# Optimization experiments

Measured on AMD Instinct MI355X. Metric: run time of the kernel, lower is better.

## Reference

```python
import jax, jax.numpy as jnp
import numpy as np

H = 2048  # hidden_size
I = 2048  # input_size
B = 2048  # batch


def setup_inputs() -> dict:
    key = jax.random.key(0)
    k0, k1, k2, k3, k4, k5 = jax.random.split(key, 6)
    # bipolar-domain activations live in [-1, 1]
    inp = jax.random.uniform(k0, (B, I), jnp.float32, minval=-1.0, maxval=1.0)
    hx = jax.random.uniform(k1, (B, H), jnp.float32, minval=-1.0, maxval=1.0)
    s = 1.0 / np.sqrt(H + I)
    w_f = jax.random.normal(k2, (H, H + I), jnp.float32) * s
    b_f = jax.random.normal(k3, (H,), jnp.float32) * s
    w_n = jax.random.normal(k4, (H, H + I), jnp.float32) * s
    b_n = jax.random.normal(k5, (H,), jnp.float32) * s
    return {"input": inp, "hx": hx, "w_f": w_f, "b_f": b_f, "w_n": w_n, "b_n": b_n}


def reference(input, hx, w_f, b_f, w_n, b_n):
    # Expected-value (probability-domain) math of the unary bitstream MGU cell.
    # fg_ug_tanh: FSULinear on [hx, x]; 'hardtanh is direct pass' -> identity act.
    fg_ug_in = jnp.concatenate([hx, input], axis=1)            # [B, H+I]
    fg_in = fg_ug_in @ w_f.T + b_f                              # [B, H]
    # fg_sigmoid: FSUAdd of [fg_in, ones] with scale=None -> (x + 1) / 2
    fg = (fg_in + 1.0) * 0.5                                    # [B, H]
    # fg_hx_mul: FSUMul with static in_1_prob = hx buffer
    fg_hx = fg * hx                                             # [B, H]
    # ng_ug_tanh: FSULinear on [fg*hx, x]
    ng_ug_in = jnp.concatenate([fg_hx, input], axis=1)          # [B, H+I]
    ng = ng_ug_in @ w_n.T + b_n                                 # [B, H]
    # fg_ng_mul: dynamic FSUMul; bipolar bit-inversion (1 - bitstream) negates value
    fg_ng = fg * ng
    # hy_add: FSUAdd([ng, -fg*ng, fg*hx], scale=1) -> plain sum
    hy = ng - fg_ng + fg_hx                                     # = (1-fg)*ng + fg*hx
    return hy
```

## Files before the change

### kernel.cpp

```cpp
#include <hip/hip_runtime.h>
#include <stdint.h>


#define Hdim 2048
#define Idim 2048
#define Bdim 2048
#define Ktot 4096
#define KHALF 2048
#define NSTEP (KHALF / 64)

typedef __bf16 bf16;
typedef __bf16 bf16x8 __attribute__((ext_vector_type(8)));
typedef float  f32x4  __attribute__((ext_vector_type(4)));

__device__ __forceinline__ void gload_lds16(const bf16* g, bf16* l) {
  __builtin_amdgcn_global_load_lds(
      (const __attribute__((address_space(1))) unsigned int*)g,
      (__attribute__((address_space(3))) unsigned int*)l,
      16, 0, 0);
}

__global__ void cvt_kernel(const float* __restrict__ src, bf16* __restrict__ dst, int n8) {
  int stride = gridDim.x * blockDim.x;
  for (int i = blockIdx.x * blockDim.x + threadIdx.x; i < n8; i += stride) {
    const float4* s = (const float4*)src + (size_t)i * 2;
    float4 a = s[0], b = s[1];
    bf16x8 o;
    o[0]=(bf16)a.x; o[1]=(bf16)a.y; o[2]=(bf16)a.z; o[3]=(bf16)a.w;
    o[4]=(bf16)b.x; o[5]=(bf16)b.y; o[6]=(bf16)b.z; o[7]=(bf16)b.w;
    *((bf16x8*)dst + i) = o;
  }
}

__global__ void build_a_kernel(const float* __restrict__ hx, const float* __restrict__ x,
                               bf16* __restrict__ A1, bf16* __restrict__ A2) {
  int stride = gridDim.x * blockDim.x;
  const int n8 = Bdim * Ktot / 8;
  for (int i = blockIdx.x * blockDim.x + threadIdx.x; i < n8; i += stride) {
    int e = i * 8;
    int b = e >> 12;
    int k = e & (Ktot - 1);
    const float* src = (k < Hdim) ? (hx + (size_t)b * Hdim + k)
                                  : (x  + (size_t)b * Idim + (k - Hdim));
    const float4* s = (const float4*)src;
    float4 va = s[0], vb = s[1];
    bf16x8 o;
    o[0]=(bf16)va.x; o[1]=(bf16)va.y; o[2]=(bf16)va.z; o[3]=(bf16)va.w;
    o[4]=(bf16)vb.x; o[5]=(bf16)vb.y; o[6]=(bf16)vb.z; o[7]=(bf16)vb.w;
    *((bf16x8*)A1 + i) = o;
    if (k >= Hdim) *((bf16x8*)A2 + i) = o;
  }
}

template<int EPI>
__global__ __launch_bounds__(512)
void gemm_kernel(const bf16* __restrict__ A, const bf16* __restrict__ W,
                 const float* __restrict__ bias,
                 const float* __restrict__ hx,
                 float* __restrict__ FG,
                 bf16* __restrict__ A2,
                 float* __restrict__ OUT)
{
  __shared__ bf16 lds[2][2][2][8192];

  int bid  = blockIdx.x;
  int sbid = (bid & 7) * 32 + (bid >> 3);
  int tm = sbid >> 4, tn = sbid & 15;

  int tid  = threadIdx.x;
  int w = tid >> 6, lane = tid & 63;
  int g = w >> 2, sub = w & 3;
  int wrow = (sub >> 1) * 64;
  int wcol = (sub & 1) * 64;
  int fr = lane & 15, fq = lane >> 4;
  int swz = fr & 7;

  int gtid = sub * 64 + lane;
  int srow = gtid >> 3;
  int csrc = (gtid & 7) ^ (srow & 7);
  const bf16* pA = A + (size_t)(tm * 128 + srow) * Ktot + csrc * 8 + g * KHALF;
  const bf16* pB = W + (size_t)(tn * 128 + srow) * Ktot + csrc * 8 + g * KHALF;
  int lbase = sub * 512;

#define STAGE(buf, koff) do {                                                      \
    _Pragma("unroll")                                                              \
    for (int jj = 0; jj < 4; ++jj) {                                               \
      gload_lds16(pA + (size_t)jj * 32 * Ktot + (koff), &lds[g][buf][0][jj * 2048 + lbase]); \
      gload_lds16(pB + (size_t)jj * 32 * Ktot + (koff), &lds[g][buf][1][jj * 2048 + lbase]); \
    }                                                                              \
  } while (0)

#define READS(buf_, j_) do {                                                       \
    int ch = (((j_) * 4 + fq) ^ swz) * 8;                                          \
    _Pragma("unroll")                                                              \
    for (int m = 0; m < 4; ++m)                                                    \
      af[m] = *(const bf16x8*)&lds[g][buf_][0][(wrow + m * 16 + fr) * 64 + ch];    \
    _Pragma("unroll")                                                              \
    for (int n = 0; n < 4; ++n)                                                    \
      bv[n] = *(const bf16x8*)&lds[g][buf_][1][(wcol + n * 16 + fr) * 64 + ch];    \
  } while (0)

  f32x4 acc[4][4] = {};

  STAGE(0, 0);

  const int NW = 2 * NSTEP + 1;
  for (int win = 0; win < NW; ++win) {
    int w2 = win - g;
    bool active = (unsigned)w2 < (unsigned)(2 * NSTEP);
    int t = w2 >> 1, j = w2 & 1, buf = t & 1;
    bf16x8 af[4], bv[4];
    if (active) {
      if (j == 1) READS(buf, 1);
      else asm volatile("s_waitcnt vmcnt(0)" ::: "memory");
    }
    __builtin_amdgcn_s_barrier();
    if (active) {
      if (j == 0) {
        READS(buf, 0);
        if (t + 1 < NSTEP) STAGE(buf ^ 1, (t + 1) * 64);
      }
      __builtin_amdgcn_s_setprio(1);
      #pragma unroll
      for (int m = 0; m < 4; ++m)
        #pragma unroll
        for (int n = 0; n < 4; ++n)
          acc[m][n] = __builtin_amdgcn_mfma_f32_16x16x32_bf16(af[m], bv[n], acc[m][n], 0, 0, 0);
      __builtin_amdgcn_s_setprio(0);
    }
  }
#undef STAGE
#undef READS

  __syncthreads();
  float* xch = (float*)&lds[0][0][0][0];
  if (g == 1) {
    #pragma unroll
    for (int m = 0; m < 4; ++m)
      #pragma unroll
      for (int n = 0; n < 4; ++n)
        *(f32x4*)&xch[sub * 4096 + (m * 4 + n) * 256 + lane * 4] = acc[m][n];
  }
  __syncthreads();
  if (g == 0) {
    int row0 = tm * 128 + wrow + fq * 4;
    int col0 = tn * 128 + wcol + fr;
    #pragma unroll
    for (int n = 0; n < 4; ++n) {
      int gcol = col0 + n * 16;
      float bv = bias[gcol];
      #pragma unroll
      for (int m = 0; m < 4; ++m) {
        f32x4 part = *(const f32x4*)&xch[sub * 4096 + (m * 4 + n) * 256 + lane * 4];
        #pragma unroll
        for (int i = 0; i < 4; ++i) {
          int grow = row0 + m * 16 + i;
          size_t idx = (size_t)grow * Hdim + gcol;
          float v = acc[m][n][i] + part[i] + bv;
          if (EPI == 0) {
            float fg   = (v + 1.0f) * 0.5f;
            float fghx = fg * hx[idx];
            FG[idx] = fg;
            A2[(size_t)grow * Ktot + gcol] = (bf16)fghx;
          } else {
            float fg   = FG[idx];
            float fghx = (float)A2[(size_t)grow * Ktot + gcol];
            OUT[idx] = v - fg * v + fghx;
          }
        }
      }
    }
  }
}

extern "C" void kernel_launch(void* const* d_in, const int* in_sizes, int n_in,
                              void* d_out, int out_size, void* d_ws, size_t ws_size,
                              hipStream_t stream) {
  const float* x   = (const float*)d_in[0];
  const float* hx  = (const float*)d_in[1];
  const float* w_f = (const float*)d_in[2];
  const float* b_f = (const float*)d_in[3];
  const float* w_n = (const float*)d_in[4];
  const float* b_n = (const float*)d_in[5];
  float* out = (float*)d_out;

  bf16* A1 = (bf16*)d_ws;
  bf16* A2 = A1 + (size_t)Bdim * Ktot;
  bf16* Wf = A2 + (size_t)Bdim * Ktot;
  bf16* Wn = Wf + (size_t)Hdim * Ktot;

  const int n8w = Hdim * Ktot / 8;
  cvt_kernel<<<1024, 256, 0, stream>>>(w_f, Wf, n8w);
  cvt_kernel<<<1024, 256, 0, stream>>>(w_n, Wn, n8w);
  build_a_kernel<<<1024, 256, 0, stream>>>(hx, x, A1, A2);

  gemm_kernel<0><<<256, 512, 0, stream>>>(A1, Wf, b_f, hx, out, A2, nullptr);
  gemm_kernel<1><<<256, 512, 0, stream>>>(A2, Wn, b_n, nullptr, out, A2, out);
}
```

Baseline: 117.9 us.

## Fuse prep kernels, drop duplicated x copy, store 1-fg as bf16

Merges the three fp32-to-bf16 conversion launches into one prep kernel. The second GEMM now reads the x half of its A operand straight from A1 instead of a duplicated copy, and reads the fg*hx half from a compact half-width buffer. The forget gate is kept as bf16 (1-fg) rather than fp32 fg, which cuts epilogue traffic and workspace. This removes two launches and several MB of writes and reads, but storing 1-fg in bf16 adds some rounding error.

```diff
diff --git a/kernel.cpp b/kernel.cpp
--- a/kernel.cpp
+++ b/kernel.cpp
@@ -20,45 +20,46 @@
       16, 0, 0);
 }
 
-__global__ void cvt_kernel(const float* __restrict__ src, bf16* __restrict__ dst, int n8) {
+__global__ void prep_kernel(const float* __restrict__ w_f, const float* __restrict__ w_n,
+                            const float* __restrict__ hx, const float* __restrict__ x,
+                            bf16* __restrict__ Wf, bf16* __restrict__ Wn,
+                            bf16* __restrict__ A1) {
+  const int n8 = Hdim * Ktot / 8;
   int stride = gridDim.x * blockDim.x;
-  for (int i = blockIdx.x * blockDim.x + threadIdx.x; i < n8; i += stride) {
-    const float4* s = (const float4*)src + (size_t)i * 2;
-    float4 a = s[0], b = s[1];
-    bf16x8 o;
-    o[0]=(bf16)a.x; o[1]=(bf16)a.y; o[2]=(bf16)a.z; o[3]=(bf16)a.w;
-    o[4]=(bf16)b.x; o[5]=(bf16)b.y; o[6]=(bf16)b.z; o[7]=(bf16)b.w;
-    *((bf16x8*)dst + i) = o;
-  }
-}
-
-__global__ void build_a_kernel(const float* __restrict__ hx, const float* __restrict__ x,
-                               bf16* __restrict__ A1, bf16* __restrict__ A2) {
-  int stride = gridDim.x * blockDim.x;
-  const int n8 = Bdim * Ktot / 8;
-  for (int i = blockIdx.x * blockDim.x + threadIdx.x; i < n8; i += stride) {
-    int e = i * 8;
-    int b = e >> 12;
-    int k = e & (Ktot - 1);
-    const float* src = (k < Hdim) ? (hx + (size_t)b * Hdim + k)
-                                  : (x  + (size_t)b * Idim + (k - Hdim));
+  for (int i = blockIdx.x * blockDim.x + threadIdx.x; i < 3 * n8; i += stride) {
+    const float* src;
+    bf16* dst;
+    if (i < n8) {
+      src = w_f + (size_t)i * 8;  dst = Wf + (size_t)i * 8;
+    } else if (i < 2 * n8) {
+      int j = i - n8;
+      src = w_n + (size_t)j * 8;  dst = Wn + (size_t)j * 8;
+    } else {
+      int j = i - 2 * n8;
+      int e = j * 8;
+      int b = e >> 12;
+      int k = e & (Ktot - 1);
+      src = (k < Hdim) ? (hx + (size_t)b * Hdim + k)
+                       : (x  + (size_t)b * Idim + (k - Hdim));
+      dst = A1 + (size_t)e;
+    }
     const float4* s = (const float4*)src;
     float4 va = s[0], vb = s[1];
     bf16x8 o;
     o[0]=(bf16)va.x; o[1]=(bf16)va.y; o[2]=(bf16)va.z; o[3]=(bf16)va.w;
     o[4]=(bf16)vb.x; o[5]=(bf16)vb.y; o[6]=(bf16)vb.z; o[7]=(bf16)vb.w;
-    *((bf16x8*)A1 + i) = o;
-    if (k >= Hdim) *((bf16x8*)A2 + i) = o;
+    *((bf16x8*)dst) = o;
   }
 }
 
 template<int EPI>
 __global__ __launch_bounds__(512)
-void gemm_kernel(const bf16* __restrict__ A, const bf16* __restrict__ W,
+void gemm_kernel(const bf16* __restrict__ A1, const bf16* __restrict__ A2L,
+                 const bf16* __restrict__ W,
                  const float* __restrict__ bias,
                  const float* __restrict__ hx,
-                 float* __restrict__ FG,
-                 bf16* __restrict__ A2,
+                 bf16* __restrict__ OMF,
+                 bf16* __restrict__ A2Lw,
                  float* __restrict__ OUT)
 {
   __shared__ bf16 lds[2][2][2][8192];
@@ -78,14 +79,26 @@
   int gtid = sub * 64 + lane;
   int srow = gtid >> 3;
   int csrc = (gtid & 7) ^ (srow & 7);
-  const bf16* pA = A + (size_t)(tm * 128 + srow) * Ktot + csrc * 8 + g * KHALF;
+
+  const bf16* pA;
+  size_t strA;
+  if (EPI == 0) {
+    pA = A1 + (size_t)(tm * 128 + srow) * Ktot + csrc * 8 + g * KHALF;
+    strA = Ktot;
+  } else if (g == 0) {
+    pA = A2L + (size_t)(tm * 128 + srow) * KHALF + csrc * 8;
+    strA = KHALF;
+  } else {
+    pA = A1 + (size_t)(tm * 128 + srow) * Ktot + csrc * 8 + Hdim;
+    strA = Ktot;
+  }
   const bf16* pB = W + (size_t)(tn * 128 + srow) * Ktot + csrc * 8 + g * KHALF;
   int lbase = sub * 512;
 
 #define STAGE(buf, koff) do {                                                      \
     _Pragma("unroll")                                                              \
     for (int jj = 0; jj < 4; ++jj) {                                               \
-      gload_lds16(pA + (size_t)jj * 32 * Ktot + (koff), &lds[g][buf][0][jj * 2048 + lbase]); \
+      gload_lds16(pA + (size_t)jj * 32 * strA + (koff), &lds[g][buf][0][jj * 2048 + lbase]); \
       gload_lds16(pB + (size_t)jj * 32 * Ktot + (koff), &lds[g][buf][1][jj * 2048 + lbase]); \
     }                                                                              \
   } while (0)
@@ -160,12 +173,12 @@
           if (EPI == 0) {
             float fg   = (v + 1.0f) * 0.5f;
             float fghx = fg * hx[idx];
-            FG[idx] = fg;
-            A2[(size_t)grow * Ktot + gcol] = (bf16)fghx;
+            OMF[idx]  = (bf16)(1.0f - fg);
+            A2Lw[(size_t)grow * KHALF + gcol] = (bf16)fghx;
           } else {
-            float fg   = FG[idx];
-            float fghx = (float)A2[(size_t)grow * Ktot + gcol];
-            OUT[idx] = v - fg * v + fghx;
+            float omf  = (float)OMF[idx];
+            float fghx = (float)A2L[idx];
+            OUT[idx] = omf * v + fghx;
           }
         }
       }
@@ -184,16 +197,14 @@
   const float* b_n = (const float*)d_in[5];
   float* out = (float*)d_out;
 
-  bf16* A1 = (bf16*)d_ws;
-  bf16* A2 = A1 + (size_t)Bdim * Ktot;
-  bf16* Wf = A2 + (size_t)Bdim * Ktot;
-  bf16* Wn = Wf + (size_t)Hdim * Ktot;
-
-  const int n8w = Hdim * Ktot / 8;
-  cvt_kernel<<<1024, 256, 0, stream>>>(w_f, Wf, n8w);
-  cvt_kernel<<<1024, 256, 0, stream>>>(w_n, Wn, n8w);
-  build_a_kernel<<<1024, 256, 0, stream>>>(hx, x, A1, A2);
-
-  gemm_kernel<0><<<256, 512, 0, stream>>>(A1, Wf, b_f, hx, out, A2, nullptr);
-  gemm_kernel<1><<<256, 512, 0, stream>>>(A2, Wn, b_n, nullptr, out, A2, out);
-}
+  bf16* A1  = (bf16*)d_ws;
+  bf16* A2L = A1  + (size_t)Bdim * Ktot;
+  bf16* Wf  = A2L + (size_t)Bdim * KHALF;
+  bf16* Wn  = Wf  + (size_t)Hdim * Ktot;
+  bf16* OMF = Wn  + (size_t)Hdim * Ktot;
+
+  prep_kernel<<<2048, 256, 0, stream>>>(w_f, w_n, hx, x, Wf, Wn, A1);
+
+  gemm_kernel<0><<<256, 512, 0, stream>>>(A1, nullptr, Wf, b_f, hx, OMF, A2L, nullptr);
+  gemm_kernel<1><<<256, 512, 0, stream>>>(A1, A2L, Wn, b_n, nullptr, OMF, nullptr, out);
+}
```

Measured after the change: 115.9 us. Within noise of the previous version (-1.7%).
